# Performance work log

Measured on AMD Instinct MI355X. Metric: run time of the kernel, lower is better.

Reference implementation:

```python
import jax, jax.numpy as jnp
import numpy as np

# LIF dynamics constants (match init_kwargs)
STEPS = 20          # T // dt
DT = 1.0
TAU_M = 20.0
TAU_S = 5.0
THRESH = 1.0
SUR_ALPHA = 10.0    # surrogate-gradient sharpness (stand-in for custom spikeprop bwd)

@jax.custom_vjp
def spike_fn(v):
    # Heaviside threshold; nondifferentiable, custom vjp supplies surrogate grad
    return (v >= THRESH).astype(v.dtype)

def _spike_fwd(v):
    return spike_fn(v), v

def _spike_bwd(v, g):
    # fast-sigmoid (SuperSpike) surrogate derivative centered at threshold
    sur = 1.0 / (1.0 + SUR_ALPHA * jnp.abs(v - THRESH)) ** 2
    return (g * sur,)

spike_fn.defvjp(_spike_fwd, _spike_bwd)


def setup_inputs() -> dict:
    key = jax.random.key(0)
    k1, k2 = jax.random.split(key)
    # Bernoulli(0.1) rate-coded input spike train: [steps, batch, input_dim]
    x = (jax.random.uniform(k1, (STEPS, 512, 2048)) < 0.1).astype(jnp.float32)
    # nn.init.normal_(weight, mean=mu, std=mu) with mu=0.1; W: [output_dim, input_dim]
    W = 0.1 + 0.1 * jax.random.normal(k2, (2048, 2048), dtype=jnp.float32)
    return {"x": x, "W": W}


def reference(x, W):
    # x: [steps, batch, input_dim] spikes; W: [out, in]
    a_m = 1.0 - DT / TAU_M   # membrane decay
    a_s = 1.0 - DT / TAU_S   # synaptic decay
    B = x.shape[1]
    O = W.shape[0]

    def step(carry, x_t):
        V, I = carry                       # [B, O] each
        V_new = a_m * V + (DT / TAU_M) * I # leaky integration of synaptic current
        s = spike_fn(V_new)                # threshold crossing -> spikes
        V_new = V_new * (1.0 - s)          # reset-to-zero on spike
        I_new = a_s * I + x_t @ W.T        # synaptic current driven by input spikes
        return (V_new, I_new), s

    init = (jnp.zeros((B, O), x.dtype), jnp.zeros((B, O), x.dtype))
    _, spikes = jax.lax.scan(step, init, x)
    return spikes  # [steps, batch, output_dim]
```

## Files before the change

### kernel.cpp

```cpp
#include <hip/hip_runtime.h>
#include <stdint.h>


#define STEPS  20
#define BATCH  512
#define DIM    2048

#define XQ_OFF   0ULL
#define WQ_OFF   20971520ULL
#define C_OFF    37748736ULL

#define GLOBAL_AS __attribute__((address_space(1)))
#define LDS_AS    __attribute__((address_space(3)))

typedef int v4i  __attribute__((ext_vector_type(4)));
typedef int v16i __attribute__((ext_vector_type(16)));


__global__ __launch_bounds__(256)
void prep_x_kernel(const float* __restrict__ x, char* __restrict__ wsb)
{
    const int bid = blockIdx.x;
    const int kc = bid & 31, mt = bid >> 5;
    const int tid = threadIdx.x;
    char* outb = wsb + (size_t)bid * 8192;
#pragma unroll
    for (int it = 0; it < 8; ++it) {
        const int idx = it * 256 + tid;
        const int mm = idx >> 4;
        const int kk4 = (idx & 15) << 2;
        const float4 v = *reinterpret_cast<const float4*>(
            x + (size_t)(mt * 128 + mm) * DIM + kc * 64 + kk4);
        uchar4 o;
        o.x = (v.x != 0.0f); o.y = (v.y != 0.0f);
        o.z = (v.z != 0.0f); o.w = (v.w != 0.0f);
        *reinterpret_cast<uchar4*>(
            outb + (((kk4 >> 4) * 128 + mm) << 4) + (kk4 & 15)) = o;
    }
}

__global__ __launch_bounds__(256)
void prep_w_kernel(const float* __restrict__ W, char* __restrict__ wsb)
{
    __shared__ __align__(16) char pl[4][8192];
    const int bid = blockIdx.x;
    const int kc = bid & 31, nt = bid >> 5;
    const int tid = threadIdx.x;
    char* wqb = wsb + WQ_OFF;
#pragma unroll
    for (int it = 0; it < 8; ++it) {
        const int idx = it * 256 + tid;
        const int nn = idx >> 4;
        const int kk4 = (idx & 15) << 2;
        const float4 v = *reinterpret_cast<const float4*>(
            W + (size_t)(nt * 128 + nn) * DIM + kc * 64 + kk4);
        int dg[4][4];
        const float* vp = &v.x;
#pragma unroll
        for (int c = 0; c < 4; ++c) {
            long long q = __double2ll_rn((double)vp[c] * 2147483648.0);
#pragma unroll
            for (int j = 0; j < 3; ++j) {
                int d = (int)(q & 255);
                if (d >= 128) d -= 256;
                dg[c][j] = d;
                q = (q - d) >> 8;
            }
            dg[c][3] = (int)q;
        }
        const int sub = (((kk4 >> 4) * 128 + nn) << 4) + (kk4 & 15);
#pragma unroll
        for (int j = 0; j < 4; ++j) {
            uchar4 o;
            o.x = (unsigned char)(dg[0][j] & 255);
            o.y = (unsigned char)(dg[1][j] & 255);
            o.z = (unsigned char)(dg[2][j] & 255);
            o.w = (unsigned char)(dg[3][j] & 255);
            *reinterpret_cast<uchar4*>(&pl[j][sub]) = o;
        }
    }
    __syncthreads();
#pragma unroll
    for (int j = 0; j < 4; ++j) {
        char* dst = wqb + ((size_t)((j * 16 + nt) * 32 + kc)) * 8192;
#pragma unroll
        for (int rep = 0; rep < 2; ++rep) {
            const int off = (rep * 256 + tid) * 16;
            *reinterpret_cast<int4*>(dst + off) =
                *reinterpret_cast<const int4*>(&pl[j][off]);
        }
    }
}

__global__ __launch_bounds__(512, 4)
void gemm_i8_kernel(const char* __restrict__ wsb_c, short* __restrict__ cp,
                    int nt0, int ntc_cnt, int no)
{
    __shared__ __align__(16) char lds[3][24576];

    const int bid = blockIdx.x;
    const int mtb = bid % 40;
    const int rest = bid / 40;
    const int ntc = rest % ntc_cnt;
    const int limb = rest / ntc_cnt;

    const int tid = threadIdx.x;
    const int lane = tid & 63, w = tid >> 6;
    const int kh = lane >> 5, ln = lane & 31;
    const int wy = w & 3, wx = w >> 2;

    const char* abase0 = wsb_c + XQ_OFF + ((size_t)(2 * mtb) * 32) * 8192;
    const char* abase1 = abase0 + (size_t)32 * 8192;
    const char* bbase = wsb_c + WQ_OFF
        + ((size_t)((limb * 16 + nt0 + ntc) * 32)) * 8192;

    const int atile = (wy >> 1) * 8192;
    const int aoffl = ((kh * 128) + (wy & 1) * 64 + ln) << 4;
    const int boff  = ((kh * 128) + wx * 64 + ln) << 4;
    const int stg = w * 1024 + (lane << 4);

    v16i acc00, acc01, acc10, acc11;
#pragma unroll
    for (int r = 0; r < 16; ++r) {
        acc00[r] = 0; acc01[r] = 0; acc10[r] = 0; acc11[r] = 0;
    }

    LDS_AS char* const lb0 = (LDS_AS char*)(&lds[0][0]);
    LDS_AS char* const lb1 = (LDS_AS char*)(&lds[1][0]);
    LDS_AS char* const lb2 = (LDS_AS char*)(&lds[2][0]);

#define STAGE(dstp, kcv) do {                                               \
        const size_t src_ = (size_t)(kcv) * 8192 + stg;                     \
        __builtin_amdgcn_global_load_lds(                                   \
            (const GLOBAL_AS void*)(abase0 + src_),                         \
            (LDS_AS void*)((dstp) + w * 1024), 16, 0, 0);                   \
        __builtin_amdgcn_global_load_lds(                                   \
            (const GLOBAL_AS void*)(abase1 + src_),                         \
            (LDS_AS void*)((dstp) + 8192 + w * 1024), 16, 0, 0);            \
        __builtin_amdgcn_global_load_lds(                                   \
            (const GLOBAL_AS void*)(bbase + src_),                          \
            (LDS_AS void*)((dstp) + 16384 + w * 1024), 16, 0, 0);           \
    } while (0)

    STAGE(lb0, 0);
    STAGE(lb1, 1);

    int cur = 0;
    for (int kc = 0; kc < 32; ++kc) {
        if (kc < 31) {
            asm volatile("s_waitcnt vmcnt(3) lgkmcnt(0)" ::: "memory");
        } else {
            asm volatile("s_waitcnt vmcnt(0) lgkmcnt(0)" ::: "memory");
        }
        __builtin_amdgcn_s_barrier();
        __builtin_amdgcn_sched_barrier(0);
        if (kc + 2 < 32) {
            int pf = cur + 2; if (pf >= 3) pf -= 3;
            LDS_AS char* pdst = (pf == 0) ? lb0 : (pf == 1) ? lb1 : lb2;
            STAGE(pdst, kc + 2);
        }
        const char* A = (const char*)(&lds[cur][atile]);
        const char* B = (const char*)(&lds[cur][16384]);
#pragma unroll
        for (int s = 0; s < 2; ++s) {
            const v4i a0 = *reinterpret_cast<const v4i*>(A + aoffl + s * 4096);
            const v4i a1 = *reinterpret_cast<const v4i*>(A + aoffl + 512 + s * 4096);
            const v4i b0 = *reinterpret_cast<const v4i*>(B + boff + s * 4096);
            const v4i b1 = *reinterpret_cast<const v4i*>(B + boff + 512 + s * 4096);
            acc00 = __builtin_amdgcn_mfma_i32_32x32x32_i8(a0, b0, acc00, 0, 0, 0);
            acc01 = __builtin_amdgcn_mfma_i32_32x32x32_i8(a0, b1, acc01, 0, 0, 0);
            acc10 = __builtin_amdgcn_mfma_i32_32x32x32_i8(a1, b0, acc10, 0, 0, 0);
            acc11 = __builtin_amdgcn_mfma_i32_32x32x32_i8(a1, b1, acc11, 0, 0, 0);
        }
        ++cur; if (cur == 3) cur = 0;
    }
#undef STAGE

    short* cpl = cp + (size_t)limb * 10240 * no;
    const int m_base = mtb * 256 + wy * 64;
    const int o_base = ntc * 128 + wx * 64 + ln;
#pragma unroll
    for (int r = 0; r < 16; ++r) {
        const int row = (r & 3) + ((r >> 2) << 3) + (kh << 2);
        const size_t m0 = (size_t)(m_base + row) * no;
        const size_t m1 = (size_t)(m_base + 32 + row) * no;
        cpl[m0 + o_base]      = (short)acc00[r];
        cpl[m0 + o_base + 32] = (short)acc01[r];
        cpl[m1 + o_base]      = (short)acc10[r];
        cpl[m1 + o_base + 32] = (short)acc11[r];
    }
}

__global__ __launch_bounds__(256)
void lif_kernel(const short* __restrict__ cp, float* __restrict__ out,
                int o0, int no, int shift)
{
    const int g = blockIdx.x * 256 + threadIdx.x;
    const int b = g >> shift;
    const int oq = g & ((1 << shift) - 1);
    const int o_local = oq << 2;
    const size_t plane = (size_t)10240 * no;

    const double A_M = 1.0 - 1.0 / 20.0;
    const double DTM = 1.0 / 20.0;
    const double A_S = 1.0 - 1.0 / 5.0;
    double V[4], I[4];
#pragma unroll
    for (int u = 0; u < 4; ++u) { V[u] = 0.0; I[u] = 0.0; }

#pragma unroll
    for (int t = 0; t < STEPS; ++t) {
        const size_t ix = (size_t)(t * BATCH + b) * no + o_local;
        const short4 c0 = *reinterpret_cast<const short4*>(cp + ix);
        const short4 c1 = *reinterpret_cast<const short4*>(cp + plane + ix);
        const short4 c2 = *reinterpret_cast<const short4*>(cp + 2 * plane + ix);
        const short4 c3 = *reinterpret_cast<const short4*>(cp + 3 * plane + ix);
        const short* p0 = &c0.x; const short* p1 = &c1.x;
        const short* p2 = &c2.x; const short* p3 = &c3.x;
        float4 s;
        float* sp = &s.x;
#pragma unroll
        for (int u = 0; u < 4; ++u) {
            const long long tot = (long long)p0[u]
                + ((long long)p1[u] << 8)
                + ((long long)p2[u] << 16)
                + ((long long)p3[u] << 24);
            const double val = (double)tot * 4.6566128730773926e-10;
            V[u] = A_M * V[u] + DTM * I[u];
            float sv = 0.0f;
            if (V[u] >= 1.0) { sv = 1.0f; V[u] = 0.0; }
            sp[u] = sv;
            I[u] = A_S * I[u] + val;
        }
        *reinterpret_cast<float4*>(
            out + (size_t)(t * BATCH + b) * DIM + o0 + o_local) = s;
    }
}


#define B_TILE 2
#define O_TILE 256
#define NT     512
#define KT     32
#define NSLAB  (DIM / KT)
#define ROWB   1024

__global__ __launch_bounds__(256)
void transpose_kernel(const float* __restrict__ W, float* __restrict__ WT)
{
    __shared__ float tile[64][65];
    const int tid = threadIdx.x;
    const int c4 = (tid & 15) * 4;
    const int rr = tid >> 4;
    const int k0 = blockIdx.x * 64, o0 = blockIdx.y * 64;
#pragma unroll
    for (int i = 0; i < 64; i += 16) {
        const float4 v = *reinterpret_cast<const float4*>(
            W + (size_t)(o0 + rr + i) * DIM + k0 + c4);
        tile[c4 + 0][rr + i] = v.x;
        tile[c4 + 1][rr + i] = v.y;
        tile[c4 + 2][rr + i] = v.z;
        tile[c4 + 3][rr + i] = v.w;
    }
    __syncthreads();
#pragma unroll
    for (int i = 0; i < 64; i += 16) {
        float4 v;
        v.x = tile[rr + i][c4 + 0];
        v.y = tile[rr + i][c4 + 1];
        v.z = tile[rr + i][c4 + 2];
        v.w = tile[rr + i][c4 + 3];
        *reinterpret_cast<float4*>(
            WT + (size_t)(k0 + rr + i) * DIM + o0 + c4) = v;
    }
}

__global__ __launch_bounds__(NT, 6)
void snn_lif_kernel(const float* __restrict__ x,
                    const float* __restrict__ WT,
                    float* __restrict__ out)
{
    __shared__ __align__(16) float wlds[(KT * ROWB) / 4];

    const int tid  = threadIdx.x;
    const int lane = tid & 63;
    const int w    = tid >> 6;
    const int bl   = w & 1;
    const int tq   = w >> 1;
    const int o_blk = blockIdx.x & 7;
    const int b_blk = blockIdx.x >> 3;
    const int b  = b_blk * B_TILE + bl;
    const int o0 = o_blk * O_TILE;

    double acc[5][4];
#pragma unroll
    for (int tt = 0; tt < 5; ++tt)
#pragma unroll
        for (int u = 0; u < 4; ++u) acc[tt][u] = 0.0;

    const int kl = lane & 31;
    float xr[5];
#pragma unroll
    for (int m = 0; m < 5; ++m)
        xr[m] = x[((size_t)(tq * 5 + m) * BATCH + b) * DIM + kl];

    const char*   gb   = (const char*)wlds + (lane << 4);
    LDS_AS char*  ldsb = (LDS_AS char*)wlds;
    const float*  wsrc = WT + o0 + (lane << 2);

    for (int kt = 0; kt < NSLAB; ++kt) {
        const int k0 = kt * KT;
        __syncthreads();
#pragma unroll
        for (int it = 0; it < 4; ++it) {
            const int r = w + it * 8;
            __builtin_amdgcn_global_load_lds(
                (const GLOBAL_AS void*)(wsrc + (size_t)(k0 + r) * DIM),
                (LDS_AS void*)(ldsb + r * ROWB), 16, 0, 0);
        }
        unsigned mk[5];
#pragma unroll
        for (int m = 0; m < 5; ++m)
            mk[m] = (unsigned)__ballot(xr[m] != 0.0f);
        __syncthreads();
        if (kt + 1 < NSLAB) {
            const int k1 = k0 + KT;
#pragma unroll
            for (int m = 0; m < 5; ++m)
                xr[m] = x[((size_t)(tq * 5 + m) * BATCH + b) * DIM + k1 + kl];
        }
#pragma unroll
        for (int m = 0; m < 5; ++m) {
            unsigned msk = mk[m];
            while (msk & (msk - 1)) {
                const int r0 = __builtin_ctz(msk); msk &= msk - 1;
                const int r1 = __builtin_ctz(msk); msk &= msk - 1;
                const float4 va = *reinterpret_cast<const float4*>(gb + (r0 << 10));
                const float4 vb = *reinterpret_cast<const float4*>(gb + (r1 << 10));
                acc[m][0] += (double)va.x; acc[m][1] += (double)va.y;
                acc[m][2] += (double)va.z; acc[m][3] += (double)va.w;
                acc[m][0] += (double)vb.x; acc[m][1] += (double)vb.y;
                acc[m][2] += (double)vb.z; acc[m][3] += (double)vb.w;
            }
            if (msk) {
                const int r = __builtin_ctz(msk);
                const float4 wv = *reinterpret_cast<const float4*>(gb + (r << 10));
                acc[m][0] += (double)wv.x; acc[m][1] += (double)wv.y;
                acc[m][2] += (double)wv.z; acc[m][3] += (double)wv.w;
            }
        }
    }

    const double A_M = 1.0 - 1.0 / 20.0;
    const double DTM = 1.0 / 20.0;
    const double A_S = 1.0 - 1.0 / 5.0;

    __syncthreads();
    double2* hand = reinterpret_cast<double2*>(wlds);
    const int hbase = bl * 256 + (lane << 2);
    const size_t obase = (size_t)o0 + (lane << 2);

    for (int seg = 0; seg < 4; ++seg) {
        if (tq == seg) {
            double V[4], I[4];
            if (seg == 0) {
#pragma unroll
                for (int u = 0; u < 4; ++u) { V[u] = 0.0; I[u] = 0.0; }
            } else {
#pragma unroll
                for (int u = 0; u < 4; ++u) {
                    const double2 h = hand[hbase + u];
                    V[u] = h.x; I[u] = h.y;
                }
            }
#pragma unroll
            for (int tt = 0; tt < 5; ++tt) {
                const int t = seg * 5 + tt;
                float4 s;
                float* sp = &s.x;
#pragma unroll
                for (int u = 0; u < 4; ++u) {
                    V[u] = A_M * V[u] + DTM * I[u];
                    float sv = 0.0f;
                    if (V[u] >= 1.0) { sv = 1.0f; V[u] = 0.0; }
                    sp[u] = sv;
                    I[u] = A_S * I[u] + acc[tt][u];
                }
                *reinterpret_cast<float4*>(
                    out + ((size_t)t * BATCH + b) * DIM + obase) = s;
            }
            if (seg < 3) {
#pragma unroll
                for (int u = 0; u < 4; ++u)
                    hand[hbase + u] = make_double2(V[u], I[u]);
            }
        }
        __syncthreads();
    }
}


extern "C" void kernel_launch(void* const* d_in, const int* in_sizes, int n_in,
                              void* d_out, int out_size, void* d_ws, size_t ws_size,
                              hipStream_t stream) {
    const float* x = (const float*)d_in[0];
    const float* W = (const float*)d_in[1];
    float* out = (float*)d_out;
    char* wsb = (char*)d_ws;

    int no = 0, shift = 0;
    if      (ws_size >= C_OFF + 81920ULL * 2048) { no = 2048; shift = 9; }
    else if (ws_size >= C_OFF + 81920ULL * 1024) { no = 1024; shift = 8; }
    else if (ws_size >= C_OFF + 81920ULL * 512)  { no = 512;  shift = 7; }
    else if (ws_size >= C_OFF + 81920ULL * 256)  { no = 256;  shift = 6; }
    else if (ws_size >= C_OFF + 81920ULL * 128)  { no = 128;  shift = 5; }

    if (no) {
        prep_x_kernel<<<2560, 256, 0, stream>>>(x, wsb);
        prep_w_kernel<<<512, 256, 0, stream>>>(W, wsb);
        short* cp = (short*)(wsb + C_OFF);
        const int ntc_cnt = no / 128;
        for (int nt0 = 0; nt0 < 16; nt0 += ntc_cnt) {
            gemm_i8_kernel<<<40 * ntc_cnt * 4, 512, 0, stream>>>(
                (const char*)wsb, cp, nt0, ntc_cnt, no);
            lif_kernel<<<no / 2, 256, 0, stream>>>(
                (const short*)cp, out, nt0 * 128, no, shift);
        }
    } else {
        float* WT = (float*)d_ws;
        dim3 tb(256);
        dim3 tg(DIM / 64, DIM / 64);
        transpose_kernel<<<tg, tb, 0, stream>>>(W, WT);
        const int grid = (BATCH / B_TILE) * (DIM / O_TILE);
        snn_lif_kernel<<<grid, NT, 0, stream>>>(x, WT, out);
    }
}
```

Before: 343.7 us.

## Switch int8 GEMM from triple to double LDS buffering with mid-step barrier

Cuts the GEMM's LDS buffers from three to two (72KB to 48KB per block), so more blocks can be resident per CU. To keep this safe, each k-step now loads all its LDS fragments into registers, waits, and passes a second barrier before issuing the prefetch that overwrites the same buffer, then runs the second half of the MFMAs. The cost is an extra barrier per k-step and less distance between a prefetch and its use, which may expose global-load latency.

```diff
diff --git a/kernel.cpp b/kernel.cpp
--- a/kernel.cpp
+++ b/kernel.cpp
@@ -96,7 +96,7 @@
 void gemm_i8_kernel(const char* __restrict__ wsb_c, short* __restrict__ cp,
                     int nt0, int ntc_cnt, int no)
 {
-    __shared__ __align__(16) char lds[3][24576];
+    __shared__ __align__(16) char lds[2][24576];
 
     const int bid = blockIdx.x;
     const int mtb = bid % 40;
@@ -127,7 +127,6 @@
 
     LDS_AS char* const lb0 = (LDS_AS char*)(&lds[0][0]);
     LDS_AS char* const lb1 = (LDS_AS char*)(&lds[1][0]);
-    LDS_AS char* const lb2 = (LDS_AS char*)(&lds[2][0]);
 
 #define STAGE(dstp, kcv) do {                                               \
         const size_t src_ = (size_t)(kcv) * 8192 + stg;                     \
@@ -142,38 +141,46 @@
             (LDS_AS void*)((dstp) + 16384 + w * 1024), 16, 0, 0);           \
     } while (0)
 
+#define KSTEP(kcv, CUR) do {                                                 \
+        if ((kcv) == 31) {                                                   \
+            asm volatile("s_waitcnt vmcnt(0) lgkmcnt(0)" ::: "memory");      \
+        } else {                                                             \
+            asm volatile("s_waitcnt vmcnt(3) lgkmcnt(0)" ::: "memory");      \
+        }                                                                    \
+        __builtin_amdgcn_s_barrier();                                        \
+        asm volatile("" ::: "memory");                                       \
+        const char* A_ = (const char*)(&lds[(CUR)][atile]);                  \
+        const char* B_ = (const char*)(&lds[(CUR)][16384]);                  \
+        const v4i a0_ = *reinterpret_cast<const v4i*>(A_ + aoffl);           \
+        const v4i a1_ = *reinterpret_cast<const v4i*>(A_ + aoffl + 512);     \
+        const v4i b0_ = *reinterpret_cast<const v4i*>(B_ + boff);            \
+        const v4i b1_ = *reinterpret_cast<const v4i*>(B_ + boff + 512);      \
+        acc00 = __builtin_amdgcn_mfma_i32_32x32x32_i8(a0_, b0_, acc00,0,0,0);\
+        acc01 = __builtin_amdgcn_mfma_i32_32x32x32_i8(a0_, b1_, acc01,0,0,0);\
+        acc10 = __builtin_amdgcn_mfma_i32_32x32x32_i8(a1_, b0_, acc10,0,0,0);\
+        acc11 = __builtin_amdgcn_mfma_i32_32x32x32_i8(a1_, b1_, acc11,0,0,0);\
+        const v4i a2_ = *reinterpret_cast<const v4i*>(A_ + aoffl + 4096);    \
+        const v4i a3_ = *reinterpret_cast<const v4i*>(A_ + aoffl + 4608);    \
+        const v4i b2_ = *reinterpret_cast<const v4i*>(B_ + boff + 4096);     \
+        const v4i b3_ = *reinterpret_cast<const v4i*>(B_ + boff + 4608);     \
+        asm volatile("s_waitcnt lgkmcnt(0)" ::: "memory");                   \
+        __builtin_amdgcn_s_barrier();                                        \
+        asm volatile("" ::: "memory");                                       \
+        if ((kcv) + 2 < 32) STAGE((CUR) ? lb1 : lb0, (kcv) + 2);             \
+        acc00 = __builtin_amdgcn_mfma_i32_32x32x32_i8(a2_, b2_, acc00,0,0,0);\
+        acc01 = __builtin_amdgcn_mfma_i32_32x32x32_i8(a2_, b3_, acc01,0,0,0);\
+        acc10 = __builtin_amdgcn_mfma_i32_32x32x32_i8(a3_, b2_, acc10,0,0,0);\
+        acc11 = __builtin_amdgcn_mfma_i32_32x32x32_i8(a3_, b3_, acc11,0,0,0);\
+    } while (0)
+
     STAGE(lb0, 0);
     STAGE(lb1, 1);
 
-    int cur = 0;
-    for (int kc = 0; kc < 32; ++kc) {
-        if (kc < 31) {
-            asm volatile("s_waitcnt vmcnt(3) lgkmcnt(0)" ::: "memory");
-        } else {
-            asm volatile("s_waitcnt vmcnt(0) lgkmcnt(0)" ::: "memory");
-        }
-        __builtin_amdgcn_s_barrier();
-        __builtin_amdgcn_sched_barrier(0);
-        if (kc + 2 < 32) {
-            int pf = cur + 2; if (pf >= 3) pf -= 3;
-            LDS_AS char* pdst = (pf == 0) ? lb0 : (pf == 1) ? lb1 : lb2;
-            STAGE(pdst, kc + 2);
-        }
-        const char* A = (const char*)(&lds[cur][atile]);
-        const char* B = (const char*)(&lds[cur][16384]);
-#pragma unroll
-        for (int s = 0; s < 2; ++s) {
-            const v4i a0 = *reinterpret_cast<const v4i*>(A + aoffl + s * 4096);
-            const v4i a1 = *reinterpret_cast<const v4i*>(A + aoffl + 512 + s * 4096);
-            const v4i b0 = *reinterpret_cast<const v4i*>(B + boff + s * 4096);
-            const v4i b1 = *reinterpret_cast<const v4i*>(B + boff + 512 + s * 4096);
-            acc00 = __builtin_amdgcn_mfma_i32_32x32x32_i8(a0, b0, acc00, 0, 0, 0);
-            acc01 = __builtin_amdgcn_mfma_i32_32x32x32_i8(a0, b1, acc01, 0, 0, 0);
-            acc10 = __builtin_amdgcn_mfma_i32_32x32x32_i8(a1, b0, acc10, 0, 0, 0);
-            acc11 = __builtin_amdgcn_mfma_i32_32x32x32_i8(a1, b1, acc11, 0, 0, 0);
-        }
-        ++cur; if (cur == 3) cur = 0;
-    }
+    for (int kc = 0; kc < 32; kc += 2) {
+        KSTEP(kc, 0);
+        KSTEP(kc + 1, 1);
+    }
+#undef KSTEP
 #undef STAGE
 
     short* cpl = cp + (size_t)limb * 10240 * no;
```

Result: faster. 331.5 us (-3.5%).
